# Kernel optimization log

Measured on AMD Instinct MI355X. Metric: run time of the kernel, lower is better.

## Reference

```python
import jax, jax.numpy as jnp
import numpy as np


def setup_inputs() -> dict:
    key = jax.random.key(0)
    ks = jax.random.split(key, 10)
    B, T, H, K = 64, 512, 1024, 49
    s = lambda fan: 1.0 / np.sqrt(fan)
    return {
        "x":       jax.random.normal(ks[0], (B, T, H), jnp.float32),
        "hiddens": jax.random.normal(ks[1], (B, T, H), jnp.float32),
        "cells":   jax.random.normal(ks[2], (B, T, H), jnp.float32),
        "V":       jax.random.normal(ks[3], (B, K, H), jnp.float32),
        "Wx":      jax.random.normal(ks[4], (H, H), jnp.float32) * s(H),
        "Whh":     jax.random.normal(ks[5], (H, H), jnp.float32) * s(H),
        "Wv":      jax.random.normal(ks[6], (K, H), jnp.float32) * s(H),
        "Wg":      jax.random.normal(ks[7], (K, H), jnp.float32) * s(H),
        "Ws":      jax.random.normal(ks[8], (K, H), jnp.float32) * s(H),
        "Wh":      jax.random.normal(ks[9], (1, K), jnp.float32) * s(K),
    }


def reference(x, hiddens, cells, V, Wx, Whh, Wv, Wg, Ws, Wh):
    # Dropout layers are identity (eval mode).
    B, T, H = x.shape
    # --- Sentinel: h0 is zeros, so the affine_h term is zero but kept for fidelity ---
    h_prev = jnp.zeros((B, H), x.dtype)
    gate = jax.nn.sigmoid(jnp.einsum('bth,oh->bto', x, Wx) + (h_prev @ Whh.T)[:, None, :])
    s_t = gate * jnp.tanh(cells)                      # [B,T,H]
    # --- Atten ---
    cv = jnp.einsum('bkh,jh->bkj', V, Wv)             # [B,49,49]
    g = jnp.einsum('bth,jh->btj', hiddens, Wg)        # [B,T,49]
    content_v = cv[:, None, :, :] + g[:, :, None, :]  # [B,T,49,49]
    z_t = jnp.einsum('btkj,j->btk', jnp.tanh(content_v), Wh[0])  # [B,T,49]
    alpha_t = jax.nn.softmax(z_t, axis=-1)            # [B,T,49]
    c_t = jnp.einsum('btk,bkh->bth', alpha_t, V)      # [B,T,H]
    content_s = jnp.einsum('bth,jh->btj', s_t, Ws) + g           # [B,T,49]
    z_ext = jnp.einsum('btj,j->bt', jnp.tanh(content_s), Wh[0])  # [B,T]
    extended = jnp.concatenate([z_t, z_ext[:, :, None]], axis=-1)  # [B,T,50]
    beta_t = jax.nn.softmax(extended, axis=-1)[:, :, -1:]          # [B,T,1]
    c_hat = beta_t * s_t + (1.0 - beta_t) * c_t
    return c_hat + hiddens
```

## Files before the change

kernel.cpp:

```cpp
#include <hip/hip_runtime.h>
#include <stdint.h>

constexpr int HD    = 1024;
constexpr int BB    = 64;
constexpr int TT    = 512;
constexpr int MR    = BB * TT;
constexpr int KA    = 49;

using bf16x8 = __attribute__((ext_vector_type(8))) short;
using f32x4  = __attribute__((ext_vector_type(4))) float;

__device__ __forceinline__ unsigned f2bf1(float f) {
    unsigned u = __builtin_bit_cast(unsigned, f);
    return (u + 0x7FFFu + ((u >> 16) & 1u)) >> 16;
}
__device__ __forceinline__ unsigned pack2(float lo, float hi) {
    return (f2bf1(lo) & 0xFFFFu) | (f2bf1(hi) << 16);
}
__device__ __forceinline__ float bf2f(unsigned short s) {
    unsigned u = ((unsigned)s) << 16;
    return __builtin_bit_cast(float, u);
}
__device__ __forceinline__ float fast_rcp(float x) { return __builtin_amdgcn_rcpf(x); }
__device__ __forceinline__ float fast_tanh(float x) {
    float ax = fabsf(x);
    float e  = __expf(-2.0f * ax);
    float t  = (1.0f - e) * fast_rcp(1.0f + e);
    return copysignf(t, x);
}
__device__ __forceinline__ float fast_sigmoid(float x) {
    return fast_rcp(1.0f + __expf(-x));
}

__global__ void cv_kernel(const float* __restrict__ V, const float* __restrict__ Wv,
                          float* __restrict__ cv) {
    __shared__ float wv[7][HD];
    __shared__ float vrow[HD];
    const int b = blockIdx.x, jg = blockIdx.y;
    const int tid = threadIdx.x;
    for (int idx = tid; idx < 7 * HD; idx += 256) {
        int jj = idx >> 10;
        wv[jj][idx & (HD - 1)] = Wv[(size_t)(jg * 7 + jj) * HD + (idx & (HD - 1))];
    }
    const int w = tid >> 6, lane = tid & 63;
    for (int k = 0; k < KA; ++k) {
        __syncthreads();
        ((float4*)vrow)[tid] = ((const float4*)(V + (size_t)(b * KA + k) * HD))[tid];
        __syncthreads();
        for (int jj = w; jj < 7; jj += 4) {
            float s = 0.f;
            #pragma unroll
            for (int i = 0; i < 16; ++i)
                s += vrow[lane + 64 * i] * wv[jj][lane + 64 * i];
            #pragma unroll
            for (int off = 32; off; off >>= 1) s += __shfl_xor(s, off);
            if (lane == 0) cv[((size_t)b * KA + k) * KA + jg * 7 + jj] = s;
        }
    }
}

__global__ void vt_kernel(const float* __restrict__ V, unsigned short* __restrict__ Vt) {
    __shared__ float tile[KA][65];
    const int b = blockIdx.x, hg = blockIdx.y;
    const int tid = threadIdx.x;
    for (int idx = tid; idx < KA * 64; idx += 256) {
        int k = idx >> 6, c = idx & 63;
        tile[k][c] = V[(size_t)(b * KA + k) * HD + hg * 64 + c];
    }
    __syncthreads();
    const int c = tid & 63, kq = tid >> 6;
    unsigned short tmp[16];
    #pragma unroll
    for (int u = 0; u < 16; ++u) {
        int k = kq * 16 + u;
        float f = (k < KA) ? tile[k][c] : 0.f;
        tmp[u] = (unsigned short)f2bf1(f);
    }
    unsigned short* dst = Vt + ((size_t)b * HD + hg * 64 + c) * 64 + kq * 16;
    ((uint4*)dst)[0] = *((const uint4*)tmp);
    ((uint4*)dst)[1] = *((const uint4*)(tmp + 8));
}

__launch_bounds__(256, 2)
__global__ void gate_gemm(const float* __restrict__ x, const float* __restrict__ Wx,
                          const float* __restrict__ cells, unsigned short* __restrict__ s_t) {
    __shared__ uint4 As[128 * 8];
    __shared__ uint4 Bs[128 * 8];
    const int tid = threadIdx.x;
    const int w = tid >> 6, lane = tid & 63, quad = lane >> 4, l15 = lane & 15;
    const int n0 = blockIdx.x * 128, m0 = blockIdx.y * 128;
    const int wm = (w >> 1) * 64, wn = (w & 1) * 64;
    f32x4 acc[4][4] = {};
    for (int kt = 0; kt < HD; kt += 64) {
        __syncthreads();
        #pragma unroll
        for (int it = 0; it < 4; ++it) {
            int c = it * 256 + tid;
            int row = c >> 3, c8 = c & 7;
            const float* gp = x + (size_t)(m0 + row) * HD + kt + c8 * 8;
            float4 f0 = ((const float4*)gp)[0];
            float4 f1 = ((const float4*)gp)[1];
            uint4 v; v.x = pack2(f0.x, f0.y); v.y = pack2(f0.z, f0.w);
            v.z = pack2(f1.x, f1.y); v.w = pack2(f1.z, f1.w);
            As[row * 8 + (c8 ^ (row & 7))] = v;
        }
        #pragma unroll
        for (int it = 0; it < 4; ++it) {
            int c = it * 256 + tid;
            int row = c >> 3, c8 = c & 7;
            const float* gp = Wx + (size_t)(n0 + row) * HD + kt + c8 * 8;
            float4 f0 = ((const float4*)gp)[0];
            float4 f1 = ((const float4*)gp)[1];
            uint4 v; v.x = pack2(f0.x, f0.y); v.y = pack2(f0.z, f0.w);
            v.z = pack2(f1.x, f1.y); v.w = pack2(f1.z, f1.w);
            Bs[row * 8 + (c8 ^ (row & 7))] = v;
        }
        __syncthreads();
        #pragma unroll
        for (int kc = 0; kc < 2; ++kc) {
            bf16x8 af[4], bfr[4];
            #pragma unroll
            for (int i = 0; i < 4; ++i) {
                int r = wm + i * 16 + l15;
                af[i] = *((const bf16x8*)&As[r * 8 + ((kc * 4 + quad) ^ (r & 7))]);
            }
            #pragma unroll
            for (int j = 0; j < 4; ++j) {
                int r = wn + j * 16 + l15;
                bfr[j] = *((const bf16x8*)&Bs[r * 8 + ((kc * 4 + quad) ^ (r & 7))]);
            }
            #pragma unroll
            for (int i = 0; i < 4; ++i)
                #pragma unroll
                for (int j = 0; j < 4; ++j)
                    acc[i][j] = __builtin_amdgcn_mfma_f32_16x16x32_bf16(af[i], bfr[j], acc[i][j], 0, 0, 0);
        }
    }
    #pragma unroll
    for (int i = 0; i < 4; ++i) {
        #pragma unroll
        for (int reg = 0; reg < 4; ++reg) {
            int rowg = m0 + wm + i * 16 + quad * 4 + reg;
            const float* crow = cells + (size_t)rowg * HD;
            unsigned short* srow = s_t + (size_t)rowg * HD;
            #pragma unroll
            for (int j = 0; j < 4; ++j) {
                int colg = n0 + wn + j * 16 + l15;
                float z = acc[i][j][reg];
                float sv = fast_sigmoid(z) * fast_tanh(crow[colg]);
                srow[colg] = (unsigned short)f2bf1(sv);
            }
        }
    }
}

template <bool A_BF16>
__launch_bounds__(256, 2)
__global__ void small_gemm(const void* __restrict__ Av, const float* __restrict__ Bw,
                           float* __restrict__ outp) {
    __shared__ uint4 As[128 * 8];
    __shared__ uint4 Bs[64 * 8];
    const int tid = threadIdx.x;
    const int w = tid >> 6, lane = tid & 63, quad = lane >> 4, l15 = lane & 15;
    const int m0 = blockIdx.x * 128;
    const int wm = w * 32;
    f32x4 acc[2][4] = {};
    for (int kt = 0; kt < HD; kt += 64) {
        __syncthreads();
        #pragma unroll
        for (int it = 0; it < 4; ++it) {
            int c = it * 256 + tid;
            int row = c >> 3, c8 = c & 7;
            uint4 v;
            if (A_BF16) {
                const unsigned short* gp = ((const unsigned short*)Av) + (size_t)(m0 + row) * HD + kt + c8 * 8;
                v = ((const uint4*)gp)[0];
            } else {
                const float* gp = ((const float*)Av) + (size_t)(m0 + row) * HD + kt + c8 * 8;
                float4 f0 = ((const float4*)gp)[0];
                float4 f1 = ((const float4*)gp)[1];
                v.x = pack2(f0.x, f0.y); v.y = pack2(f0.z, f0.w);
                v.z = pack2(f1.x, f1.y); v.w = pack2(f1.z, f1.w);
            }
            As[row * 8 + (c8 ^ (row & 7))] = v;
        }
        #pragma unroll
        for (int it = 0; it < 2; ++it) {
            int c = it * 256 + tid;
            int row = c >> 3, c8 = c & 7;
            uint4 v; v.x = v.y = v.z = v.w = 0u;
            if (row < KA) {
                const float* gp = Bw + (size_t)row * HD + kt + c8 * 8;
                float4 f0 = ((const float4*)gp)[0];
                float4 f1 = ((const float4*)gp)[1];
                v.x = pack2(f0.x, f0.y); v.y = pack2(f0.z, f0.w);
                v.z = pack2(f1.x, f1.y); v.w = pack2(f1.z, f1.w);
            }
            Bs[row * 8 + (c8 ^ (row & 7))] = v;
        }
        __syncthreads();
        #pragma unroll
        for (int kc = 0; kc < 2; ++kc) {
            bf16x8 af[2], bfr[4];
            #pragma unroll
            for (int i = 0; i < 2; ++i) {
                int r = wm + i * 16 + l15;
                af[i] = *((const bf16x8*)&As[r * 8 + ((kc * 4 + quad) ^ (r & 7))]);
            }
            #pragma unroll
            for (int j = 0; j < 4; ++j) {
                int r = j * 16 + l15;
                bfr[j] = *((const bf16x8*)&Bs[r * 8 + ((kc * 4 + quad) ^ (r & 7))]);
            }
            #pragma unroll
            for (int i = 0; i < 2; ++i)
                #pragma unroll
                for (int j = 0; j < 4; ++j)
                    acc[i][j] = __builtin_amdgcn_mfma_f32_16x16x32_bf16(af[i], bfr[j], acc[i][j], 0, 0, 0);
        }
    }
    #pragma unroll
    for (int i = 0; i < 2; ++i)
        #pragma unroll
        for (int reg = 0; reg < 4; ++reg) {
            int rowg = m0 + wm + i * 16 + quad * 4 + reg;
            #pragma unroll
            for (int j = 0; j < 4; ++j)
                outp[(size_t)rowg * 64 + j * 16 + l15] = acc[i][j][reg];
        }
}

__global__ void attn_kernel(const float* __restrict__ g, const float* __restrict__ ss,
                            const float* __restrict__ cv, const float* __restrict__ Wh,
                            unsigned short* __restrict__ alpha, float* __restrict__ beta) {
    __shared__ float cvs[KA * KA];
    const int b = blockIdx.x, t0 = blockIdx.y * 64;
    const int tid = threadIdx.x, w = tid >> 6, lane = tid & 63;
    for (int idx = tid; idx < KA * KA; idx += 256)
        cvs[idx] = cv[(size_t)b * KA * KA + idx];
    const float wh_l = (lane < KA) ? Wh[lane] : 0.f;
    __syncthreads();
    for (int ti = 0; ti < 16; ++ti) {
        const int t = t0 + ti * 4 + w;
        const size_t row = (size_t)b * TT + t;
        const float gj  = g[row * 64 + lane];
        const float ssj = ss[row * 64 + lane] + gj;
        float ve = fast_tanh(ssj) * wh_l;
        #pragma unroll
        for (int off = 32; off; off >>= 1) ve += __shfl_xor(ve, off);
        float zk = 0.f;
        const float* cr = cvs + lane * KA;
        for (int j = 0; j < KA; ++j) {
            float gb = __shfl(gj, j);
            float wb = __shfl(wh_l, j);
            zk += fast_tanh(cr[j] + gb) * wb;
        }
        float zval = (lane < KA) ? zk : -1e30f;
        float M = zval;
        #pragma unroll
        for (int off = 32; off; off >>= 1) M = fmaxf(M, __shfl_xor(M, off));
        M = fmaxf(M, ve);
        float ek = (lane < KA) ? __expf(zk - M) : 0.f;
        float S = ek;
        #pragma unroll
        for (int off = 32; off; off >>= 1) S += __shfl_xor(S, off);
        float eext = __expf(ve - M);
        float bet  = eext * fast_rcp(S + eext);
        float al   = ek * fast_rcp(S);
        alpha[row * 64 + lane] = (unsigned short)f2bf1(al);
        if (lane == 0) beta[row] = bet;
    }
}

__launch_bounds__(256, 2)
__global__ void ct_final(const unsigned short* __restrict__ alpha, const unsigned short* __restrict__ Vt,
                         const unsigned short* __restrict__ s_t, const float* __restrict__ hiddens,
                         const float* __restrict__ beta, float* __restrict__ out) {
    __shared__ uint4 As[128 * 8];
    __shared__ uint4 Bs[128 * 8];
    const int tid = threadIdx.x;
    const int w = tid >> 6, lane = tid & 63, quad = lane >> 4, l15 = lane & 15;
    const int n0 = blockIdx.x * 128, m0 = blockIdx.y * 128;
    const int b = m0 >> 9;
    const int wm = (w >> 1) * 64, wn = (w & 1) * 64;
    f32x4 acc[4][4] = {};
    #pragma unroll
    for (int it = 0; it < 4; ++it) {
        int c = it * 256 + tid;
        int row = c >> 3, c8 = c & 7;
        As[row * 8 + (c8 ^ (row & 7))] = ((const uint4*)(alpha + (size_t)(m0 + row) * 64))[c8];
    }
    #pragma unroll
    for (int it = 0; it < 4; ++it) {
        int c = it * 256 + tid;
        int row = c >> 3, c8 = c & 7;
        Bs[row * 8 + (c8 ^ (row & 7))] = ((const uint4*)(Vt + ((size_t)b * HD + n0 + row) * 64))[c8];
    }
    __syncthreads();
    #pragma unroll
    for (int kc = 0; kc < 2; ++kc) {
        bf16x8 af[4], bfr[4];
        #pragma unroll
        for (int i = 0; i < 4; ++i) {
            int r = wm + i * 16 + l15;
            af[i] = *((const bf16x8*)&As[r * 8 + ((kc * 4 + quad) ^ (r & 7))]);
        }
        #pragma unroll
        for (int j = 0; j < 4; ++j) {
            int r = wn + j * 16 + l15;
            bfr[j] = *((const bf16x8*)&Bs[r * 8 + ((kc * 4 + quad) ^ (r & 7))]);
        }
        #pragma unroll
        for (int i = 0; i < 4; ++i)
            #pragma unroll
            for (int j = 0; j < 4; ++j)
                acc[i][j] = __builtin_amdgcn_mfma_f32_16x16x32_bf16(af[i], bfr[j], acc[i][j], 0, 0, 0);
    }
    #pragma unroll
    for (int i = 0; i < 4; ++i) {
        #pragma unroll
        for (int reg = 0; reg < 4; ++reg) {
            int rowg = m0 + wm + i * 16 + quad * 4 + reg;
            float bet = beta[rowg];
            const unsigned short* sr = s_t + (size_t)rowg * HD;
            const float* hr = hiddens + (size_t)rowg * HD;
            float* orow = out + (size_t)rowg * HD;
            #pragma unroll
            for (int j = 0; j < 4; ++j) {
                int colg = n0 + wn + j * 16 + l15;
                float ct = acc[i][j][reg];
                float sv = bf2f(sr[colg]);
                orow[colg] = bet * sv + (1.f - bet) * ct + hr[colg];
            }
        }
    }
}

extern "C" void kernel_launch(void* const* d_in, const int* in_sizes, int n_in,
                              void* d_out, int out_size, void* d_ws, size_t ws_size,
                              hipStream_t stream) {
    (void)in_sizes; (void)n_in; (void)out_size; (void)ws_size;
    const float* x       = (const float*)d_in[0];
    const float* hiddens = (const float*)d_in[1];
    const float* cells   = (const float*)d_in[2];
    const float* V       = (const float*)d_in[3];
    const float* Wx      = (const float*)d_in[4];
    const float* Wv      = (const float*)d_in[6];
    const float* Wg      = (const float*)d_in[7];
    const float* Ws      = (const float*)d_in[8];
    const float* Wh      = (const float*)d_in[9];
    float* out = (float*)d_out;

    char* ws = (char*)d_ws;
    unsigned short* s_t   = (unsigned short*)ws;  ws += (size_t)MR * HD * 2;
    unsigned short* alpha = (unsigned short*)ws;  ws += (size_t)MR * 64 * 2;
    unsigned short* Vt    = (unsigned short*)ws;  ws += (size_t)BB * HD * 64 * 2;
    float* gbuf = (float*)ws;                     ws += (size_t)MR * 64 * 4;
    float* ssb  = (float*)ws;                     ws += (size_t)MR * 64 * 4;
    float* cvb  = (float*)ws;                     ws += (size_t)BB * KA * KA * 4;
    float* beta = (float*)ws;                     ws += (size_t)MR * 4;

    cv_kernel<<<dim3(BB, 7),  dim3(256), 0, stream>>>(V, Wv, cvb);
    vt_kernel<<<dim3(BB, 16), dim3(256), 0, stream>>>(V, Vt);
    small_gemm<false><<<dim3(MR / 128), dim3(256), 0, stream>>>((const void*)hiddens, Wg, gbuf);
    gate_gemm<<<dim3(8, MR / 128), dim3(256), 0, stream>>>(x, Wx, cells, s_t);
    small_gemm<true><<<dim3(MR / 128), dim3(256), 0, stream>>>((const void*)s_t, Ws, ssb);
    attn_kernel<<<dim3(BB, 8), dim3(256), 0, stream>>>(gbuf, ssb, cvb, Wh, alpha, beta);
    ct_final<<<dim3(8, MR / 128), dim3(256), 0, stream>>>(alpha, Vt, s_t, hiddens, beta, out);
}
```

Baseline: 921.0 us.

## Pre-convert inputs to bf16 and stage GEMM tiles with async global-to-LDS loads

Adds conversion kernels that turn x, hiddens, Wx, Wg and Ws into bf16 up front, using the output buffer as scratch for x and hiddens. The GEMM kernels then load tiles with global_load_lds async copies instead of per-thread fp32 loads, packing and swizzled LDS stores. The LDS layout becomes unswizzled, which can cause bank conflicts. ct_final now uses narrower N tiles and stages results through LDS so the epilogue can use vectorized, coalesced stores. The trade-off is an extra full pass over x and hiddens to convert them, in exchange for halving the bytes the GEMM loops read.

New measurement: 779.4 us. -15.4%, faster.

```diff
diff --git a/kernel.cpp b/kernel.cpp
--- a/kernel.cpp
+++ b/kernel.cpp
@@ -1,14 +1,15 @@
 #include <hip/hip_runtime.h>
 #include <stdint.h>
 
-constexpr int HD    = 1024;
-constexpr int BB    = 64;
-constexpr int TT    = 512;
-constexpr int MR    = BB * TT;
-constexpr int KA    = 49;
+constexpr int HD = 1024;
+constexpr int BB = 64;
+constexpr int TT = 512;
+constexpr int MR = BB * TT;
+constexpr int KA = 49;
 
 using bf16x8 = __attribute__((ext_vector_type(8))) short;
 using f32x4  = __attribute__((ext_vector_type(4))) float;
+typedef unsigned short ushortt;
 
 __device__ __forceinline__ unsigned f2bf1(float f) {
     unsigned u = __builtin_bit_cast(unsigned, f);
@@ -31,6 +32,34 @@
 __device__ __forceinline__ float fast_sigmoid(float x) {
     return fast_rcp(1.0f + __expf(-x));
 }
+__device__ __forceinline__ void async_copy16(const void* gptr, void* ldsptr) {
+    __builtin_amdgcn_global_load_lds(
+        (const __attribute__((address_space(1))) unsigned int*)gptr,
+        (__attribute__((address_space(3))) unsigned int*)ldsptr,
+        16, 0, 0);
+}
+
+__global__ void f32_to_bf16(const float* __restrict__ in, ushortt* __restrict__ outp) {
+    int i = blockIdx.x * 256 + threadIdx.x;
+    const float4* p = (const float4*)in + (size_t)i * 2;
+    float4 f0 = p[0], f1 = p[1];
+    uint4 v; v.x = pack2(f0.x, f0.y); v.y = pack2(f0.z, f0.w);
+    v.z = pack2(f1.x, f1.y); v.w = pack2(f1.z, f1.w);
+    ((uint4*)outp)[i] = v;
+}
+
+__global__ void cvt_w49(const float* __restrict__ W, ushortt* __restrict__ outp) {
+    int i = blockIdx.x * 256 + threadIdx.x;
+    int row = i >> 7, c8 = i & 127;
+    uint4 v; v.x = v.y = v.z = v.w = 0u;
+    if (row < KA) {
+        const float4* p = (const float4*)(W + (size_t)row * HD) + c8 * 2;
+        float4 f0 = p[0], f1 = p[1];
+        v.x = pack2(f0.x, f0.y); v.y = pack2(f0.z, f0.w);
+        v.z = pack2(f1.x, f1.y); v.w = pack2(f1.z, f1.w);
+    }
+    ((uint4*)outp)[i] = v;
+}
 
 __global__ void cv_kernel(const float* __restrict__ V, const float* __restrict__ Wv,
                           float* __restrict__ cv) {
@@ -59,7 +88,7 @@
     }
 }
 
-__global__ void vt_kernel(const float* __restrict__ V, unsigned short* __restrict__ Vt) {
+__global__ void vt_kernel(const float* __restrict__ V, ushortt* __restrict__ Vt) {
     __shared__ float tile[KA][65];
     const int b = blockIdx.x, hg = blockIdx.y;
     const int tid = threadIdx.x;
@@ -69,66 +98,48 @@
     }
     __syncthreads();
     const int c = tid & 63, kq = tid >> 6;
-    unsigned short tmp[16];
+    ushortt tmp[16];
     #pragma unroll
     for (int u = 0; u < 16; ++u) {
         int k = kq * 16 + u;
         float f = (k < KA) ? tile[k][c] : 0.f;
-        tmp[u] = (unsigned short)f2bf1(f);
-    }
-    unsigned short* dst = Vt + ((size_t)b * HD + hg * 64 + c) * 64 + kq * 16;
+        tmp[u] = (ushortt)f2bf1(f);
+    }
+    ushortt* dst = Vt + ((size_t)b * HD + hg * 64 + c) * 64 + kq * 16;
     ((uint4*)dst)[0] = *((const uint4*)tmp);
     ((uint4*)dst)[1] = *((const uint4*)(tmp + 8));
 }
 
-__launch_bounds__(256, 2)
-__global__ void gate_gemm(const float* __restrict__ x, const float* __restrict__ Wx,
-                          const float* __restrict__ cells, unsigned short* __restrict__ s_t) {
-    __shared__ uint4 As[128 * 8];
-    __shared__ uint4 Bs[128 * 8];
+__launch_bounds__(256)
+__global__ void gate_gemm2(const ushortt* __restrict__ xb, const ushortt* __restrict__ Wxb,
+                           const float* __restrict__ cells, ushortt* __restrict__ s_t) {
+    __shared__ ushortt As[128 * 64];
+    __shared__ ushortt Bs[128 * 64];
     const int tid = threadIdx.x;
     const int w = tid >> 6, lane = tid & 63, quad = lane >> 4, l15 = lane & 15;
     const int n0 = blockIdx.x * 128, m0 = blockIdx.y * 128;
     const int wm = (w >> 1) * 64, wn = (w & 1) * 64;
+    const int lrow = lane >> 3, lcol = lane & 7;
     f32x4 acc[4][4] = {};
     for (int kt = 0; kt < HD; kt += 64) {
         __syncthreads();
         #pragma unroll
         for (int it = 0; it < 4; ++it) {
-            int c = it * 256 + tid;
-            int row = c >> 3, c8 = c & 7;
-            const float* gp = x + (size_t)(m0 + row) * HD + kt + c8 * 8;
-            float4 f0 = ((const float4*)gp)[0];
-            float4 f1 = ((const float4*)gp)[1];
-            uint4 v; v.x = pack2(f0.x, f0.y); v.y = pack2(f0.z, f0.w);
-            v.z = pack2(f1.x, f1.y); v.w = pack2(f1.z, f1.w);
-            As[row * 8 + (c8 ^ (row & 7))] = v;
-        }
-        #pragma unroll
-        for (int it = 0; it < 4; ++it) {
-            int c = it * 256 + tid;
-            int row = c >> 3, c8 = c & 7;
-            const float* gp = Wx + (size_t)(n0 + row) * HD + kt + c8 * 8;
-            float4 f0 = ((const float4*)gp)[0];
-            float4 f1 = ((const float4*)gp)[1];
-            uint4 v; v.x = pack2(f0.x, f0.y); v.y = pack2(f0.z, f0.w);
-            v.z = pack2(f1.x, f1.y); v.w = pack2(f1.z, f1.w);
-            Bs[row * 8 + (c8 ^ (row & 7))] = v;
+            int c = w * 4 + it;
+            int row = c * 8 + lrow;
+            async_copy16(xb  + (size_t)(m0 + row) * HD + kt + lcol * 8, (char*)As + c * 1024);
+            async_copy16(Wxb + (size_t)(n0 + row) * HD + kt + lcol * 8, (char*)Bs + c * 1024);
         }
         __syncthreads();
         #pragma unroll
         for (int kc = 0; kc < 2; ++kc) {
             bf16x8 af[4], bfr[4];
             #pragma unroll
-            for (int i = 0; i < 4; ++i) {
-                int r = wm + i * 16 + l15;
-                af[i] = *((const bf16x8*)&As[r * 8 + ((kc * 4 + quad) ^ (r & 7))]);
-            }
-            #pragma unroll
-            for (int j = 0; j < 4; ++j) {
-                int r = wn + j * 16 + l15;
-                bfr[j] = *((const bf16x8*)&Bs[r * 8 + ((kc * 4 + quad) ^ (r & 7))]);
-            }
+            for (int i = 0; i < 4; ++i)
+                af[i] = *((const bf16x8*)&As[(wm + i * 16 + l15) * 64 + kc * 32 + quad * 8]);
+            #pragma unroll
+            for (int j = 0; j < 4; ++j)
+                bfr[j] = *((const bf16x8*)&Bs[(wn + j * 16 + l15) * 64 + kc * 32 + quad * 8]);
             #pragma unroll
             for (int i = 0; i < 4; ++i)
                 #pragma unroll
@@ -142,76 +153,52 @@
         for (int reg = 0; reg < 4; ++reg) {
             int rowg = m0 + wm + i * 16 + quad * 4 + reg;
             const float* crow = cells + (size_t)rowg * HD;
-            unsigned short* srow = s_t + (size_t)rowg * HD;
+            ushortt* srow = s_t + (size_t)rowg * HD;
             #pragma unroll
             for (int j = 0; j < 4; ++j) {
                 int colg = n0 + wn + j * 16 + l15;
                 float z = acc[i][j][reg];
                 float sv = fast_sigmoid(z) * fast_tanh(crow[colg]);
-                srow[colg] = (unsigned short)f2bf1(sv);
+                srow[colg] = (ushortt)f2bf1(sv);
             }
         }
     }
 }
 
-template <bool A_BF16>
-__launch_bounds__(256, 2)
-__global__ void small_gemm(const void* __restrict__ Av, const float* __restrict__ Bw,
-                           float* __restrict__ outp) {
-    __shared__ uint4 As[128 * 8];
-    __shared__ uint4 Bs[64 * 8];
+__launch_bounds__(256)
+__global__ void small_gemm2(const ushortt* __restrict__ A, const ushortt* __restrict__ B64,
+                            float* __restrict__ outp) {
+    __shared__ ushortt As[128 * 64];
+    __shared__ ushortt Bs[64 * 64];
     const int tid = threadIdx.x;
     const int w = tid >> 6, lane = tid & 63, quad = lane >> 4, l15 = lane & 15;
-    const int m0 = blockIdx.x * 128;
-    const int wm = w * 32;
+    const int m0 = blockIdx.x * 128, wm = w * 32;
+    const int lrow = lane >> 3, lcol = lane & 7;
     f32x4 acc[2][4] = {};
     for (int kt = 0; kt < HD; kt += 64) {
         __syncthreads();
         #pragma unroll
         for (int it = 0; it < 4; ++it) {
-            int c = it * 256 + tid;
-            int row = c >> 3, c8 = c & 7;
-            uint4 v;
-            if (A_BF16) {
-                const unsigned short* gp = ((const unsigned short*)Av) + (size_t)(m0 + row) * HD + kt + c8 * 8;
-                v = ((const uint4*)gp)[0];
-            } else {
-                const float* gp = ((const float*)Av) + (size_t)(m0 + row) * HD + kt + c8 * 8;
-                float4 f0 = ((const float4*)gp)[0];
-                float4 f1 = ((const float4*)gp)[1];
-                v.x = pack2(f0.x, f0.y); v.y = pack2(f0.z, f0.w);
-                v.z = pack2(f1.x, f1.y); v.w = pack2(f1.z, f1.w);
-            }
-            As[row * 8 + (c8 ^ (row & 7))] = v;
+            int c = w * 4 + it;
+            int row = c * 8 + lrow;
+            async_copy16(A + (size_t)(m0 + row) * HD + kt + lcol * 8, (char*)As + c * 1024);
         }
         #pragma unroll
         for (int it = 0; it < 2; ++it) {
-            int c = it * 256 + tid;
-            int row = c >> 3, c8 = c & 7;
-            uint4 v; v.x = v.y = v.z = v.w = 0u;
-            if (row < KA) {
-                const float* gp = Bw + (size_t)row * HD + kt + c8 * 8;
-                float4 f0 = ((const float4*)gp)[0];
-                float4 f1 = ((const float4*)gp)[1];
-                v.x = pack2(f0.x, f0.y); v.y = pack2(f0.z, f0.w);
-                v.z = pack2(f1.x, f1.y); v.w = pack2(f1.z, f1.w);
-            }
-            Bs[row * 8 + (c8 ^ (row & 7))] = v;
+            int c = w * 2 + it;
+            int row = c * 8 + lrow;
+            async_copy16(B64 + (size_t)row * HD + kt + lcol * 8, (char*)Bs + c * 1024);
         }
         __syncthreads();
         #pragma unroll
         for (int kc = 0; kc < 2; ++kc) {
             bf16x8 af[2], bfr[4];
             #pragma unroll
-            for (int i = 0; i < 2; ++i) {
-                int r = wm + i * 16 + l15;
-                af[i] = *((const bf16x8*)&As[r * 8 + ((kc * 4 + quad) ^ (r & 7))]);
-            }
-            #pragma unroll
-            for (int j = 0; j < 4; ++j) {
-                int r = j * 16 + l15;
-                bfr[j] = *((const bf16x8*)&Bs[r * 8 + ((kc * 4 + quad) ^ (r & 7))]);
-            }
+            for (int i = 0; i < 2; ++i)
+                af[i] = *((const bf16x8*)&As[(wm + i * 16 + l15) * 64 + kc * 32 + quad * 8]);
+            #pragma unroll
+            for (int j = 0; j < 4; ++j)
+                bfr[j] = *((const bf16x8*)&Bs[(j * 16 + l15) * 64 + kc * 32 + quad * 8]);
             #pragma unroll
             for (int i = 0; i < 2; ++i)
                 #pragma unroll
@@ -232,7 +219,7 @@
 
 __global__ void attn_kernel(const float* __restrict__ g, const float* __restrict__ ss,
                             const float* __restrict__ cv, const float* __restrict__ Wh,
-                            unsigned short* __restrict__ alpha, float* __restrict__ beta) {
+                            ushortt* __restrict__ alpha, float* __restrict__ beta) {
     __shared__ float cvs[KA * KA];
     const int b = blockIdx.x, t0 = blockIdx.y * 64;
     const int tid = threadIdx.x, w = tid >> 6, lane = tid & 63;
@@ -267,72 +254,81 @@
         float eext = __expf(ve - M);
         float bet  = eext * fast_rcp(S + eext);
         float al   = ek * fast_rcp(S);
-        alpha[row * 64 + lane] = (unsigned short)f2bf1(al);
+        alpha[row * 64 + lane] = (ushortt)f2bf1(al);
         if (lane == 0) beta[row] = bet;
     }
 }
 
-__launch_bounds__(256, 2)
-__global__ void ct_final(const unsigned short* __restrict__ alpha, const unsigned short* __restrict__ Vt,
-                         const unsigned short* __restrict__ s_t, const float* __restrict__ hiddens,
-                         const float* __restrict__ beta, float* __restrict__ out) {
-    __shared__ uint4 As[128 * 8];
-    __shared__ uint4 Bs[128 * 8];
+__launch_bounds__(256)
+__global__ void ct_final2(const ushortt* __restrict__ alpha, const ushortt* __restrict__ Vt,
+                          const ushortt* __restrict__ s_t, const float* __restrict__ hiddens,
+                          const float* __restrict__ beta, float* __restrict__ outp) {
+    __shared__ __align__(16) char smem[128 * 68 * 4];
+    ushortt* As = (ushortt*)smem;
+    ushortt* Bs = (ushortt*)(smem + 16384);
+    float*   cts = (float*)smem;
     const int tid = threadIdx.x;
     const int w = tid >> 6, lane = tid & 63, quad = lane >> 4, l15 = lane & 15;
-    const int n0 = blockIdx.x * 128, m0 = blockIdx.y * 128;
+    const int n0 = blockIdx.x * 64, m0 = blockIdx.y * 128;
     const int b = m0 >> 9;
-    const int wm = (w >> 1) * 64, wn = (w & 1) * 64;
-    f32x4 acc[4][4] = {};
+    const int lrow = lane >> 3, lcol = lane & 7;
+    const int wm = w * 32;
     #pragma unroll
     for (int it = 0; it < 4; ++it) {
-        int c = it * 256 + tid;
-        int row = c >> 3, c8 = c & 7;
-        As[row * 8 + (c8 ^ (row & 7))] = ((const uint4*)(alpha + (size_t)(m0 + row) * 64))[c8];
-    }
-    #pragma unroll
-    for (int it = 0; it < 4; ++it) {
-        int c = it * 256 + tid;
-        int row = c >> 3, c8 = c & 7;
-        Bs[row * 8 + (c8 ^ (row & 7))] = ((const uint4*)(Vt + ((size_t)b * HD + n0 + row) * 64))[c8];
-    }
-    __syncthreads();
+        int c = w * 4 + it;
+        async_copy16(alpha + (size_t)(m0 + c * 8 + lrow) * 64 + lcol * 8, (char*)As + c * 1024);
+    }
+    #pragma unroll
+    for (int it = 0; it < 2; ++it) {
+        int c = w * 2 + it;
+        async_copy16(Vt + ((size_t)b * HD + n0 + c * 8 + lrow) * 64 + lcol * 8, (char*)Bs + c * 1024);
+    }
+    __syncthreads();
+    f32x4 acc[2][4] = {};
     #pragma unroll
     for (int kc = 0; kc < 2; ++kc) {
-        bf16x8 af[4], bfr[4];
-        #pragma unroll
-        for (int i = 0; i < 4; ++i) {
-            int r = wm + i * 16 + l15;
-            af[i] = *((const bf16x8*)&As[r * 8 + ((kc * 4 + quad) ^ (r & 7))]);
-        }
-        #pragma unroll
-        for (int j = 0; j < 4; ++j) {
-            int r = wn + j * 16 + l15;
-            bfr[j] = *((const bf16x8*)&Bs[r * 8 + ((kc * 4 + quad) ^ (r & 7))]);
-        }
-        #pragma unroll
-        for (int i = 0; i < 4; ++i)
+        bf16x8 af[2], bfr[4];
+        #pragma unroll
+        for (int i = 0; i < 2; ++i)
+            af[i] = *((const bf16x8*)&As[(wm + i * 16 + l15) * 64 + kc * 32 + quad * 8]);
+        #pragma unroll
+        for (int j = 0; j < 4; ++j)
+            bfr[j] = *((const bf16x8*)&Bs[(j * 16 + l15) * 64 + kc * 32 + quad * 8]);
+        #pragma unroll
+        for (int i = 0; i < 2; ++i)
             #pragma unroll
             for (int j = 0; j < 4; ++j)
                 acc[i][j] = __builtin_amdgcn_mfma_f32_16x16x32_bf16(af[i], bfr[j], acc[i][j], 0, 0, 0);
     }
-    #pragma unroll
-    for (int i = 0; i < 4; ++i) {
-        #pragma unroll
-        for (int reg = 0; reg < 4; ++reg) {
-            int rowg = m0 + wm + i * 16 + quad * 4 + reg;
-            float bet = beta[rowg];
-            const unsigned short* sr = s_t + (size_t)rowg * HD;
-            const float* hr = hiddens + (size_t)rowg * HD;
-            float* orow = out + (size_t)rowg * HD;
-            #pragma unroll
-            for (int j = 0; j < 4; ++j) {
-                int colg = n0 + wn + j * 16 + l15;
-                float ct = acc[i][j][reg];
-                float sv = bf2f(sr[colg]);
-                orow[colg] = bet * sv + (1.f - bet) * ct + hr[colg];
-            }
-        }
+    __syncthreads();
+    #pragma unroll
+    for (int i = 0; i < 2; ++i)
+        #pragma unroll
+        for (int reg = 0; reg < 4; ++reg)
+            #pragma unroll
+            for (int j = 0; j < 4; ++j)
+                cts[(wm + i * 16 + quad * 4 + reg) * 68 + j * 16 + l15] = acc[i][j][reg];
+    __syncthreads();
+    const int c8 = tid & 7, r0 = tid >> 3;
+    #pragma unroll
+    for (int r = 0; r < 4; ++r) {
+        int row = r0 + r * 32;
+        int rowg = m0 + row;
+        float bet = beta[rowg], omb = 1.f - bet;
+        const ushortt* sp = s_t + (size_t)rowg * HD + n0 + c8 * 8;
+        const float*   hp = hiddens + (size_t)rowg * HD + n0 + c8 * 8;
+        float*         op = outp + (size_t)rowg * HD + n0 + c8 * 8;
+        union { uint4 u4; ushortt us[8]; } sv;
+        sv.u4 = *((const uint4*)sp);
+        float4 h0 = ((const float4*)hp)[0], h1 = ((const float4*)hp)[1];
+        const float* cp = cts + row * 68 + c8 * 8;
+        float o[8];
+        float hh[8] = {h0.x, h0.y, h0.z, h0.w, h1.x, h1.y, h1.z, h1.w};
+        #pragma unroll
+        for (int u = 0; u < 8; ++u)
+            o[u] = bet * bf2f(sv.us[u]) + omb * cp[u] + hh[u];
+        ((float4*)op)[0] = make_float4(o[0], o[1], o[2], o[3]);
+        ((float4*)op)[1] = make_float4(o[4], o[5], o[6], o[7]);
     }
 }
 
@@ -351,20 +347,31 @@
     const float* Wh      = (const float*)d_in[9];
     float* out = (float*)d_out;
 
+    ushortt* xb = (ushortt*)d_out;
+    ushortt* hb = (ushortt*)d_out + (size_t)MR * HD;
+
     char* ws = (char*)d_ws;
-    unsigned short* s_t   = (unsigned short*)ws;  ws += (size_t)MR * HD * 2;
-    unsigned short* alpha = (unsigned short*)ws;  ws += (size_t)MR * 64 * 2;
-    unsigned short* Vt    = (unsigned short*)ws;  ws += (size_t)BB * HD * 64 * 2;
-    float* gbuf = (float*)ws;                     ws += (size_t)MR * 64 * 4;
-    float* ssb  = (float*)ws;                     ws += (size_t)MR * 64 * 4;
-    float* cvb  = (float*)ws;                     ws += (size_t)BB * KA * KA * 4;
-    float* beta = (float*)ws;                     ws += (size_t)MR * 4;
-
+    ushortt* s_t   = (ushortt*)ws;  ws += (size_t)MR * HD * 2;
+    ushortt* alpha = (ushortt*)ws;  ws += (size_t)MR * 64 * 2;
+    ushortt* Vt    = (ushortt*)ws;  ws += (size_t)BB * HD * 64 * 2;
+    float* gbuf = (float*)ws;       ws += (size_t)MR * 64 * 4;
+    float* ssb  = (float*)ws;       ws += (size_t)MR * 64 * 4;
+    float* cvb  = (float*)ws;       ws += (size_t)BB * KA * KA * 4;
+    float* beta = (float*)ws;       ws += (size_t)MR * 4;
+    ushortt* Wxb   = (ushortt*)ws;  ws += (size_t)HD * HD * 2;
+    ushortt* Wgb64 = (ushortt*)ws;  ws += (size_t)64 * HD * 2;
+    ushortt* Wsb64 = (ushortt*)ws;  ws += (size_t)64 * HD * 2;
+
+    f32_to_bf16<<<dim3(MR * HD / 8 / 256), dim3(256), 0, stream>>>(x, xb);
+    f32_to_bf16<<<dim3(MR * HD / 8 / 256), dim3(256), 0, stream>>>(hiddens, hb);
+    f32_to_bf16<<<dim3(HD * HD / 8 / 256), dim3(256), 0, stream>>>(Wx, Wxb);
+    cvt_w49<<<dim3(32), dim3(256), 0, stream>>>(Wg, Wgb64);
+    cvt_w49<<<dim3(32), dim3(256), 0, stream>>>(Ws, Wsb64);
     cv_kernel<<<dim3(BB, 7),  dim3(256), 0, stream>>>(V, Wv, cvb);
     vt_kernel<<<dim3(BB, 16), dim3(256), 0, stream>>>(V, Vt);
-    small_gemm<false><<<dim3(MR / 128), dim3(256), 0, stream>>>((const void*)hiddens, Wg, gbuf);
-    gate_gemm<<<dim3(8, MR / 128), dim3(256), 0, stream>>>(x, Wx, cells, s_t);
-    small_gemm<true><<<dim3(MR / 128), dim3(256), 0, stream>>>((const void*)s_t, Ws, ssb);
+    small_gemm2<<<dim3(MR / 128), dim3(256), 0, stream>>>(hb, Wgb64, gbuf);
+    gate_gemm2<<<dim3(8, MR / 128), dim3(256), 0, stream>>>(xb, Wxb, cells, s_t);
+    small_gemm2<<<dim3(MR / 128), dim3(256), 0, stream>>>(s_t, Wsb64, ssb);
     attn_kernel<<<dim3(BB, 8), dim3(256), 0, stream>>>(gbuf, ssb, cvb, Wh, alpha, beta);
-    ct_final<<<dim3(8, MR / 128), dim3(256), 0, stream>>>(alpha, Vt, s_t, hiddens, beta, out);
-}
+    ct_final2<<<dim3(16, MR / 128), dim3(256), 0, stream>>>(alpha, Vt, s_t, hiddens, beta, out);
+}
```
